# Kernel optimization log

Hardware: AMD Instinct MI355X
Metric: run time of the kernel (lower is better)

## Reference

```python
import jax, jax.numpy as jnp
import numpy as np

D_MODEL = 1024

def setup_inputs() -> dict:
    key = jax.random.key(0)
    kx, kq, kk, kv, ko = jax.random.split(key, 5)
    B, S, D = 8, 2048, D_MODEL
    scale = 1.0 / np.sqrt(D)
    x = jax.random.normal(kx, (B, S, D), dtype=jnp.float32)
    # nn.Linear weights are [out, in]; y = x @ W.T
    Wq = jax.random.normal(kq, (D, D), dtype=jnp.float32) * scale
    Wk = jax.random.normal(kk, (D, D), dtype=jnp.float32) * scale
    Wv = jax.random.normal(kv, (D, D), dtype=jnp.float32) * scale
    Wo = jax.random.normal(ko, (D, D), dtype=jnp.float32) * scale
    return {"x": x, "Wq": Wq, "Wk": Wk, "Wv": Wv, "Wo": Wo}

def reference(x, Wq, Wk, Wv, Wo):
    # Single-head self-attention, dropout in eval mode (identity).
    d_model = x.shape[-1]
    q = jnp.einsum('bsd,ed->bse', x, Wq)
    k = jnp.einsum('bsd,ed->bse', x, Wk)
    v = jnp.einsum('bsd,ed->bse', x, Wv)
    scores = jnp.einsum('bqe,bke->bqk', q, k) / jnp.sqrt(jnp.float32(d_model))
    attn = jax.nn.softmax(scores, axis=-1)
    weighted = jnp.einsum('bqk,bke->bqe', attn, v)
    return jnp.einsum('bqe,oe->bqo', weighted, Wo)
```

## Files before the change

### kernel.cpp

```cpp
#include <hip/hip_runtime.h>
#include <hip/hip_bf16.h>
#include <stdint.h>

typedef short bf16x8 __attribute__((ext_vector_type(8)));
typedef float f32x4 __attribute__((ext_vector_type(4)));

__device__ __forceinline__ unsigned short f2bf(float x) {
  uint32_t u = __builtin_bit_cast(uint32_t, x);
  u += 0x7FFFu + ((u >> 16) & 1u);
  return (unsigned short)(u >> 16);
}
__device__ __forceinline__ float bf2f(unsigned short u) {
  uint32_t v = ((uint32_t)u) << 16;
  return __builtin_bit_cast(float, v);
}

__device__ __forceinline__ void gl2lds16(const void* g, void* l) {
  __builtin_amdgcn_global_load_lds(
      (const __attribute__((address_space(1))) unsigned int*)g,
      (__attribute__((address_space(3))) unsigned int*)l, 16, 0, 0);
}

__global__ __launch_bounds__(256) void cast_f32_bf16_k(
    const float* __restrict__ s, unsigned short* __restrict__ d, long n) {
  long i = ((long)blockIdx.x * 256 + threadIdx.x) * 8;
  if (i >= n) return;
  float4 a = *(const float4*)(s + i);
  float4 b = *(const float4*)(s + i + 4);
  bf16x8 o;
  o[0] = (short)f2bf(a.x); o[1] = (short)f2bf(a.y);
  o[2] = (short)f2bf(a.z); o[3] = (short)f2bf(a.w);
  o[4] = (short)f2bf(b.x); o[5] = (short)f2bf(b.y);
  o[6] = (short)f2bf(b.z); o[7] = (short)f2bf(b.w);
  *(bf16x8*)(d + i) = o;
}

__global__ __launch_bounds__(256) void cast4_f32_bf16_k(
    const float* __restrict__ s0, const float* __restrict__ s1,
    const float* __restrict__ s2, const float* __restrict__ s3,
    unsigned short* __restrict__ d, long n) {
  const float* s = blockIdx.z == 0 ? s0 : blockIdx.z == 1 ? s1 : blockIdx.z == 2 ? s2 : s3;
  long i = ((long)blockIdx.x * 256 + threadIdx.x) * 8;
  if (i >= n) return;
  float4 a = *(const float4*)(s + i);
  float4 b = *(const float4*)(s + i + 4);
  bf16x8 o;
  o[0] = (short)f2bf(a.x); o[1] = (short)f2bf(a.y);
  o[2] = (short)f2bf(a.z); o[3] = (short)f2bf(a.w);
  o[4] = (short)f2bf(b.x); o[5] = (short)f2bf(b.y);
  o[6] = (short)f2bf(b.z); o[7] = (short)f2bf(b.w);
  *(bf16x8*)(d + blockIdx.z * n + i) = o;
}

template <typename OutT>
__global__ __launch_bounds__(512, 2) void gemm_bt8(
    const unsigned short* __restrict__ A, const unsigned short* __restrict__ B,
    OutT* __restrict__ C, int M, int N, int K,
    long sA, long sB, long sC, float alpha) {
  extern __shared__ __align__(16) char smem[];
  const int bz = blockIdx.z;
  const int gx = gridDim.x;
  const int nwg = gx * gridDim.y;
  const int idx = blockIdx.y * gx + blockIdx.x;
  const int wg = (idx & 7) * (nwg >> 3) + (idx >> 3);
  const int bm = wg / gx, bn = wg % gx;

  const int tid = threadIdx.x, lane = tid & 63, wave = tid >> 6;
  const int wm = wave >> 2, wn = wave & 3;

  const char* Ac = (const char*)(A + (long)bz * sA + (long)bm * 256 * K);
  const char* Bc = (const char*)(B + (long)bz * sB + (long)bn * 256 * K);
  C += (long)bz * sC;
  const long ld = (long)K * 2;

  int srow[2], scol[2];
#pragma unroll
  for (int c = 0; c < 2; ++c) {
    int d = ((wave << 1 | c) << 10) + (lane << 4);
    int p = d ^ (((d >> 6) & 3) << 4);
    srow[c] = p >> 6; scol[c] = p & 63;
  }

  auto stageReg = [&](int dstbuf, int op, int kh, const char* gbase, int ktb) {
    char* reg = smem + (((dstbuf << 1 | op) << 1 | kh) << 14);
#pragma unroll
    for (int c = 0; c < 2; ++c) {
      gl2lds16(gbase + (long)srow[c] * ld + (ktb + kh * 64 + scol[c]),
               reg + ((wave << 1 | c) << 10) + (lane << 4));
    }
  };

  const int colx = (((lane >> 4) ^ (lane & 3)) << 4);
  const int rbA = (wm * 128 + (lane & 15)) * 64;
  const int rbB = (wn * 64 + (lane & 15)) * 64;

#pragma unroll
  for (int ph = 0; ph < 4; ++ph)
    stageReg(0, ph & 1, ph >> 1, (ph & 1) ? Bc : Ac, 0);
  asm volatile("s_waitcnt vmcnt(4)" ::: "memory");
  __builtin_amdgcn_s_barrier();
  __builtin_amdgcn_sched_barrier(0);

  f32x4 acc[8][4] = {};
  bf16x8 bfr[4];
  const int nt = K >> 6;
  for (int t = 0; t < nt; ++t) {
    const int b = t & 1;
    const int ktb = (t + 1 < nt ? t + 1 : 0) << 7;
#pragma unroll
    for (int ph = 0; ph < 4; ++ph) {
      const int g = ph & 1, kh = ph >> 1;
      stageReg(b ^ 1, ph & 1, ph >> 1, (ph & 1) ? Bc : Ac, ktb);
      const char* regA = smem + (((b << 1 | 0) << 1 | kh) << 14);
      const char* regB = smem + (((b << 1 | 1) << 1 | kh) << 14);
      bf16x8 afr[4];
#pragma unroll
      for (int m = 0; m < 4; ++m)
        afr[m] = *(const bf16x8*)(regA + rbA + g * 4096 + m * 1024 + colx);
      if (g == 0) {
#pragma unroll
        for (int n = 0; n < 4; ++n)
          bfr[n] = *(const bf16x8*)(regB + rbB + n * 1024 + colx);
      }
      __builtin_amdgcn_s_barrier();
      asm volatile("s_waitcnt lgkmcnt(0)" ::: "memory");
      __builtin_amdgcn_sched_barrier(0);
      __builtin_amdgcn_s_setprio(1);
#pragma unroll
      for (int m = 0; m < 4; ++m)
#pragma unroll
        for (int n = 0; n < 4; ++n)
          acc[g * 4 + m][n] = __builtin_amdgcn_mfma_f32_16x16x32_bf16(
              afr[m], bfr[n], acc[g * 4 + m][n], 0, 0, 0);
      __builtin_amdgcn_s_setprio(0);
      asm volatile("s_waitcnt vmcnt(4)" ::: "memory");
      __builtin_amdgcn_s_barrier();
      __builtin_amdgcn_sched_barrier(0);
    }
  }

  const long row0 = (long)bm * 256 + wm * 128 + (lane >> 4) * 4;
  const int col0 = bn * 256 + wn * 64 + (lane & 15);
#pragma unroll
  for (int m = 0; m < 8; ++m) {
#pragma unroll
    for (int n = 0; n < 4; ++n) {
#pragma unroll
      for (int r = 0; r < 4; ++r) {
        long row = row0 + m * 16 + r;
        int col = col0 + n * 16;
        float v = acc[m][n][r] * alpha;
        if constexpr (sizeof(OutT) == 2)
          C[row * (long)N + col] = (OutT)f2bf(v);
        else
          C[row * (long)N + col] = v;
      }
    }
  }
}

__global__ __launch_bounds__(256) void softmax_inplace(unsigned short* __restrict__ s, int C) {
  __shared__ float red[8];
  long row = blockIdx.x;
  unsigned short* p = s + row * (long)C;
  int tid = threadIdx.x, lane = tid & 63, w = tid >> 6;
  bf16x8 raw = *(const bf16x8*)(p + tid * 8);
  float v[8];
  float mx = -3.4e38f;
#pragma unroll
  for (int j = 0; j < 8; ++j) { v[j] = bf2f((unsigned short)raw[j]); mx = fmaxf(mx, v[j]); }
#pragma unroll
  for (int o = 32; o > 0; o >>= 1) mx = fmaxf(mx, __shfl_xor(mx, o));
  if (lane == 0) red[w] = mx;
  __syncthreads();
  mx = fmaxf(fmaxf(red[0], red[1]), fmaxf(red[2], red[3]));
  float sum = 0.f;
#pragma unroll
  for (int j = 0; j < 8; ++j) { v[j] = __expf(v[j] - mx); sum += v[j]; }
#pragma unroll
  for (int o = 32; o > 0; o >>= 1) sum += __shfl_xor(sum, o);
  if (lane == 0) red[4 + w] = sum;
  __syncthreads();
  float inv = 1.f / (red[4] + red[5] + red[6] + red[7]);
  bf16x8 o8;
#pragma unroll
  for (int j = 0; j < 8; ++j) o8[j] = (short)f2bf(v[j] * inv);
  *(bf16x8*)(p + tid * 8) = o8;
}

__global__ __launch_bounds__(256) void transpose_bf16(
    const unsigned short* __restrict__ in, unsigned short* __restrict__ out, int R, int C) {
  __shared__ unsigned short t[32][33];
  long b = blockIdx.z;
  in += b * (long)R * C; out += b * (long)R * C;
  int c0 = blockIdx.x * 32, r0 = blockIdx.y * 32;
  int tx = threadIdx.x & 31, ty = threadIdx.x >> 5;
#pragma unroll
  for (int i = 0; i < 4; ++i)
    t[ty + i * 8][tx] = in[(long)(r0 + ty + i * 8) * C + c0 + tx];
  __syncthreads();
#pragma unroll
  for (int i = 0; i < 4; ++i)
    out[(long)(c0 + ty + i * 8) * R + r0 + tx] = t[tx][ty + i * 8];
}

extern "C" void kernel_launch(void* const* d_in, const int* in_sizes, int n_in,
                              void* d_out, int out_size, void* d_ws, size_t ws_size,
                              hipStream_t stream) {
  (void)in_sizes; (void)n_in; (void)out_size; (void)ws_size;
  const float* x  = (const float*)d_in[0];
  const float* Wq = (const float*)d_in[1];
  const float* Wk = (const float*)d_in[2];
  const float* Wv = (const float*)d_in[3];
  const float* Wo = (const float*)d_in[4];
  const int B = 8, S = 2048, D = 1024;
  const long MB = 1 << 20;
  char* w = (char*)d_ws;
  unsigned short* Wqb = (unsigned short*)(w + 0 * MB);
  unsigned short* Wkb = (unsigned short*)(w + 2 * MB);
  unsigned short* Wvb = (unsigned short*)(w + 4 * MB);
  unsigned short* Wob = (unsigned short*)(w + 6 * MB);
  unsigned short* xb  = (unsigned short*)(w + 8 * MB);
  unsigned short* qb  = (unsigned short*)(w + 40 * MB);
  unsigned short* kb  = (unsigned short*)(w + 72 * MB);
  unsigned short* vb  = (unsigned short*)(w + 104 * MB);
  unsigned short* vt  = qb;
  unsigned short* wb  = xb;
  unsigned short* attn = (unsigned short*)d_out;
  float* out = (float*)d_out;

  long nx = (long)B * S * D;
  long nw = (long)D * D;

  const int LDSB = 131072;
  hipFuncSetAttribute((const void*)gemm_bt8<unsigned short>,
                      hipFuncAttributeMaxDynamicSharedMemorySize, LDSB);
  hipFuncSetAttribute((const void*)gemm_bt8<float>,
                      hipFuncAttributeMaxDynamicSharedMemorySize, LDSB);

  cast_f32_bf16_k<<<(int)(nx / 2048), 256, 0, stream>>>(x, xb, nx);
  dim3 gW((int)(nw / 2048), 1, 4);
  cast4_f32_bf16_k<<<gW, 256, 0, stream>>>(Wq, Wk, Wv, Wo, Wqb, nw);

  dim3 gP(D / 256, (B * S) / 256, 1);
  gemm_bt8<unsigned short><<<gP, 512, LDSB, stream>>>(xb, Wqb, qb, B * S, D, D, 0, 0, 0, 1.f);
  gemm_bt8<unsigned short><<<gP, 512, LDSB, stream>>>(xb, Wkb, kb, B * S, D, D, 0, 0, 0, 1.f);
  gemm_bt8<unsigned short><<<gP, 512, LDSB, stream>>>(xb, Wvb, vb, B * S, D, D, 0, 0, 0, 1.f);

  dim3 gS(S / 256, S / 256, B);
  gemm_bt8<unsigned short><<<gS, 512, LDSB, stream>>>(qb, kb, attn, S, S, D,
      (long)S * D, (long)S * D, (long)S * S, 0.03125f);

  dim3 gT(D / 32, S / 32, B);
  transpose_bf16<<<gT, 256, 0, stream>>>(vb, vt, S, D);

  softmax_inplace<<<B * S, 256, 0, stream>>>(attn, S);

  dim3 gPV(D / 256, S / 256, B);
  gemm_bt8<unsigned short><<<gPV, 512, LDSB, stream>>>(attn, vt, wb, S, D, S,
      (long)S * S, (long)D * S, (long)S * D, 1.f);

  gemm_bt8<float><<<gP, 512, LDSB, stream>>>(wb, Wob, out, B * S, D, D, 0, 0, 0, 1.f);
}
```

Before: 365.3 us.

## Fuse V transpose into projection epilogue and restructure LDS staging layout

```diff
diff --git a/kernel.cpp b/kernel.cpp
--- a/kernel.cpp
+++ b/kernel.cpp
@@ -52,7 +52,7 @@
   *(bf16x8*)(d + blockIdx.z * n + i) = o;
 }
 
-template <typename OutT>
+template <typename OutT, bool TRANSV>
 __global__ __launch_bounds__(512, 2) void gemm_bt8(
     const unsigned short* __restrict__ A, const unsigned short* __restrict__ B,
     OutT* __restrict__ C, int M, int N, int K,
@@ -73,31 +73,25 @@
   C += (long)bz * sC;
   const long ld = (long)K * 2;
 
-  int srow[2], scol[2];
-#pragma unroll
-  for (int c = 0; c < 2; ++c) {
-    int d = ((wave << 1 | c) << 10) + (lane << 4);
-    int p = d ^ (((d >> 6) & 3) << 4);
-    srow[c] = p >> 6; scol[c] = p & 63;
-  }
-
-  auto stageReg = [&](int dstbuf, int op, int kh, const char* gbase, int ktb) {
-    char* reg = smem + (((dstbuf << 1 | op) << 1 | kh) << 14);
-#pragma unroll
-    for (int c = 0; c < 2; ++c) {
-      gl2lds16(gbase + (long)srow[c] * ld + (ktb + kh * 64 + scol[c]),
-               reg + ((wave << 1 | c) << 10) + (lane << 4));
-    }
+  const int sr = tid >> 3;
+  const int scol = (((tid & 7) ^ ((tid >> 3) & 7)) << 4);
+
+  auto stageChunk = [&](int buf, int op, int c, const char* gbase, int ktb) {
+    char* reg = smem + ((buf * 2 + op) << 15);
+    gl2lds16(gbase + (long)(sr + c * 64) * ld + (ktb + scol),
+             reg + c * 8192 + tid * 16);
   };
 
-  const int colx = (((lane >> 4) ^ (lane & 3)) << 4);
-  const int rbA = (wm * 128 + (lane & 15)) * 64;
-  const int rbB = (wn * 64 + (lane & 15)) * 64;
-
-#pragma unroll
-  for (int ph = 0; ph < 4; ++ph)
-    stageReg(0, ph & 1, ph >> 1, (ph & 1) ? Bc : Ac, 0);
-  asm volatile("s_waitcnt vmcnt(4)" ::: "memory");
+  const int colx0 = ((lane >> 4) << 4) ^ ((lane & 7) << 4);
+  const int colx1 = (64 | ((lane >> 4) << 4)) ^ ((lane & 7) << 4);
+  const int rbA = (wm * 128 + (lane & 15)) * 128;
+  const int rbB = (wn * 64 + (lane & 15)) * 128;
+
+#pragma unroll
+  for (int c = 0; c < 4; ++c) stageChunk(0, 0, c, Ac, 0);
+#pragma unroll
+  for (int c = 0; c < 4; ++c) stageChunk(0, 1, c, Bc, 0);
+  asm volatile("s_waitcnt vmcnt(0)" ::: "memory");
   __builtin_amdgcn_s_barrier();
   __builtin_amdgcn_sched_barrier(0);
 
@@ -110,17 +104,19 @@
 #pragma unroll
     for (int ph = 0; ph < 4; ++ph) {
       const int g = ph & 1, kh = ph >> 1;
-      stageReg(b ^ 1, ph & 1, ph >> 1, (ph & 1) ? Bc : Ac, ktb);
-      const char* regA = smem + (((b << 1 | 0) << 1 | kh) << 14);
-      const char* regB = smem + (((b << 1 | 1) << 1 | kh) << 14);
+      const int colx = kh ? colx1 : colx0;
+      stageChunk(b ^ 1, ph >> 1, (ph & 1) * 2 + 0, (ph >> 1) ? Bc : Ac, ktb);
+      stageChunk(b ^ 1, ph >> 1, (ph & 1) * 2 + 1, (ph >> 1) ? Bc : Ac, ktb);
+      const char* regA = smem + ((b * 2 + 0) << 15);
+      const char* regB = smem + ((b * 2 + 1) << 15);
       bf16x8 afr[4];
 #pragma unroll
       for (int m = 0; m < 4; ++m)
-        afr[m] = *(const bf16x8*)(regA + rbA + g * 4096 + m * 1024 + colx);
+        afr[m] = *(const bf16x8*)(regA + rbA + g * (64 * 128) + m * (16 * 128) + colx);
       if (g == 0) {
 #pragma unroll
         for (int n = 0; n < 4; ++n)
-          bfr[n] = *(const bf16x8*)(regB + rbB + n * 1024 + colx);
+          bfr[n] = *(const bf16x8*)(regB + rbB + n * (16 * 128) + colx);
       }
       __builtin_amdgcn_s_barrier();
       asm volatile("s_waitcnt lgkmcnt(0)" ::: "memory");
@@ -133,7 +129,7 @@
           acc[g * 4 + m][n] = __builtin_amdgcn_mfma_f32_16x16x32_bf16(
               afr[m], bfr[n], acc[g * 4 + m][n], 0, 0, 0);
       __builtin_amdgcn_s_setprio(0);
-      asm volatile("s_waitcnt vmcnt(4)" ::: "memory");
+      if (ph == 3) asm volatile("s_waitcnt vmcnt(0)" ::: "memory");
       __builtin_amdgcn_s_barrier();
       __builtin_amdgcn_sched_barrier(0);
     }
@@ -145,15 +141,24 @@
   for (int m = 0; m < 8; ++m) {
 #pragma unroll
     for (int n = 0; n < 4; ++n) {
-#pragma unroll
-      for (int r = 0; r < 4; ++r) {
-        long row = row0 + m * 16 + r;
-        int col = col0 + n * 16;
-        float v = acc[m][n][r] * alpha;
-        if constexpr (sizeof(OutT) == 2)
-          C[row * (long)N + col] = (OutT)f2bf(v);
-        else
-          C[row * (long)N + col] = v;
+      if constexpr (TRANSV) {
+        long row = row0 + m * 16;
+        long base = ((row >> 11) << 21) + ((long)(col0 + n * 16) << 11) + (row & 2047);
+        ushort4 st;
+        st.x = f2bf(acc[m][n][0]); st.y = f2bf(acc[m][n][1]);
+        st.z = f2bf(acc[m][n][2]); st.w = f2bf(acc[m][n][3]);
+        *(ushort4*)((unsigned short*)C + base) = st;
+      } else {
+#pragma unroll
+        for (int r = 0; r < 4; ++r) {
+          long row = row0 + m * 16 + r;
+          int col = col0 + n * 16;
+          float v = acc[m][n][r] * alpha;
+          if constexpr (sizeof(OutT) == 2)
+            C[row * (long)N + col] = (OutT)f2bf(v);
+          else
+            C[row * (long)N + col] = v;
+        }
       }
     }
   }
@@ -186,22 +191,6 @@
 #pragma unroll
   for (int j = 0; j < 8; ++j) o8[j] = (short)f2bf(v[j] * inv);
   *(bf16x8*)(p + tid * 8) = o8;
-}
-
-__global__ __launch_bounds__(256) void transpose_bf16(
-    const unsigned short* __restrict__ in, unsigned short* __restrict__ out, int R, int C) {
-  __shared__ unsigned short t[32][33];
-  long b = blockIdx.z;
-  in += b * (long)R * C; out += b * (long)R * C;
-  int c0 = blockIdx.x * 32, r0 = blockIdx.y * 32;
-  int tx = threadIdx.x & 31, ty = threadIdx.x >> 5;
-#pragma unroll
-  for (int i = 0; i < 4; ++i)
-    t[ty + i * 8][tx] = in[(long)(r0 + ty + i * 8) * C + c0 + tx];
-  __syncthreads();
-#pragma unroll
-  for (int i = 0; i < 4; ++i)
-    out[(long)(c0 + ty + i * 8) * R + r0 + tx] = t[tx][ty + i * 8];
 }
 
 extern "C" void kernel_launch(void* const* d_in, const int* in_sizes, int n_in,
@@ -223,8 +212,7 @@
   unsigned short* xb  = (unsigned short*)(w + 8 * MB);
   unsigned short* qb  = (unsigned short*)(w + 40 * MB);
   unsigned short* kb  = (unsigned short*)(w + 72 * MB);
-  unsigned short* vb  = (unsigned short*)(w + 104 * MB);
-  unsigned short* vt  = qb;
+  unsigned short* vt  = (unsigned short*)(w + 104 * MB);
   unsigned short* wb  = xb;
   unsigned short* attn = (unsigned short*)d_out;
   float* out = (float*)d_out;
@@ -233,9 +221,11 @@
   long nw = (long)D * D;
 
   const int LDSB = 131072;
-  hipFuncSetAttribute((const void*)gemm_bt8<unsigned short>,
+  hipFuncSetAttribute((const void*)gemm_bt8<unsigned short, false>,
                       hipFuncAttributeMaxDynamicSharedMemorySize, LDSB);
-  hipFuncSetAttribute((const void*)gemm_bt8<float>,
+  hipFuncSetAttribute((const void*)gemm_bt8<unsigned short, true>,
+                      hipFuncAttributeMaxDynamicSharedMemorySize, LDSB);
+  hipFuncSetAttribute((const void*)gemm_bt8<float, false>,
                       hipFuncAttributeMaxDynamicSharedMemorySize, LDSB);
 
   cast_f32_bf16_k<<<(int)(nx / 2048), 256, 0, stream>>>(x, xb, nx);
@@ -243,22 +233,19 @@
   cast4_f32_bf16_k<<<gW, 256, 0, stream>>>(Wq, Wk, Wv, Wo, Wqb, nw);
 
   dim3 gP(D / 256, (B * S) / 256, 1);
-  gemm_bt8<unsigned short><<<gP, 512, LDSB, stream>>>(xb, Wqb, qb, B * S, D, D, 0, 0, 0, 1.f);
-  gemm_bt8<unsigned short><<<gP, 512, LDSB, stream>>>(xb, Wkb, kb, B * S, D, D, 0, 0, 0, 1.f);
-  gemm_bt8<unsigned short><<<gP, 512, LDSB, stream>>>(xb, Wvb, vb, B * S, D, D, 0, 0, 0, 1.f);
+  gemm_bt8<unsigned short, false><<<gP, 512, LDSB, stream>>>(xb, Wqb, qb, B * S, D, D, 0, 0, 0, 1.f);
+  gemm_bt8<unsigned short, false><<<gP, 512, LDSB, stream>>>(xb, Wkb, kb, B * S, D, D, 0, 0, 0, 1.f);
+  gemm_bt8<unsigned short, true><<<gP, 512, LDSB, stream>>>(xb, Wvb, vt, B * S, D, D, 0, 0, 0, 1.f);
 
   dim3 gS(S / 256, S / 256, B);
-  gemm_bt8<unsigned short><<<gS, 512, LDSB, stream>>>(qb, kb, attn, S, S, D,
+  gemm_bt8<unsigned short, false><<<gS, 512, LDSB, stream>>>(qb, kb, attn, S, S, D,
       (long)S * D, (long)S * D, (long)S * S, 0.03125f);
 
-  dim3 gT(D / 32, S / 32, B);
-  transpose_bf16<<<gT, 256, 0, stream>>>(vb, vt, S, D);
-
   softmax_inplace<<<B * S, 256, 0, stream>>>(attn, S);
 
   dim3 gPV(D / 256, S / 256, B);
-  gemm_bt8<unsigned short><<<gPV, 512, LDSB, stream>>>(attn, vt, wb, S, D, S,
+  gemm_bt8<unsigned short, false><<<gPV, 512, LDSB, stream>>>(attn, vt, wb, S, D, S,
       (long)S * S, (long)D * S, (long)S * D, 1.f);
 
-  gemm_bt8<float><<<gP, 512, LDSB, stream>>>(wb, Wob, out, B * S, D, D, 0, 0, 0, 1.f);
-}
+  gemm_bt8<float, false><<<gP, 512, LDSB, stream>>>(wb, Wob, out, B * S, D, D, 0, 0, 0, 1.f);
+}
```

New measurement: 346.5 us. 1.05x faster.
